# Optimization experiments

Hardware: AMD Instinct MI355X
Metric: run time of the kernel (lower is better)

Reference implementation:

```python
import jax, jax.numpy as jnp
import numpy as np

N_HEAD, N_KV, HEAD_DIM, GATE_CH = 16, 4, 128, 32

def _rope(x, cos, sin):
    d = x.shape[3] // 2
    x1, x2 = x[..., :d], x[..., d:]
    return jnp.concatenate([x1 * cos + x2 * sin, x1 * (-sin) + x2 * cos], axis=3)

def _rmsnorm(x):
    xf = x.astype(jnp.float32)
    return (x * jax.lax.rsqrt(jnp.mean(xf * xf, axis=-1, keepdims=True) + 1e-6)).astype(x.dtype)

def setup_inputs() -> dict:
    key = jax.random.key(0)
    ks = jax.random.split(key, 9)
    B, T, C = 2, 2048, 2048
    return {
        "x":  jax.random.normal(ks[0], (B, T, C), jnp.float32),
        "ve": jax.random.normal(ks[1], (B, T, N_KV * HEAD_DIM), jnp.float32),
        "cos": jax.random.uniform(ks[2], (T, 1, HEAD_DIM // 2), jnp.float32),
        "sin": jax.random.uniform(ks[3], (T, 1, HEAD_DIM // 2), jnp.float32),
        "Wq": jax.random.normal(ks[4], (C, N_HEAD * HEAD_DIM), jnp.float32) * 0.02,
        "Wk": jax.random.normal(ks[5], (C, N_KV * HEAD_DIM), jnp.float32) * 0.02,
        "Wv": jax.random.normal(ks[6], (C, N_KV * HEAD_DIM), jnp.float32) * 0.02,
        "Wg": jax.random.normal(ks[7], (GATE_CH, N_KV), jnp.float32) * 0.02,
        "Wo": jax.random.normal(ks[8], (C, C), jnp.float32) * 0.02,
        "window": 1024,
    }

def reference(x, ve, cos, sin, Wq, Wk, Wv, Wg, Wo, window):
    B, T, C = x.shape
    q = (x @ Wq).reshape(B, T, N_HEAD, HEAD_DIM)
    k = (x @ Wk).reshape(B, T, N_KV, HEAD_DIM)
    v = (x @ Wv).reshape(B, T, N_KV, HEAD_DIM)
    # value-embedding gate (ve_gate active for this layer)
    gate = 2.0 * jax.nn.sigmoid(x[..., :GATE_CH] @ Wg)  # (B,T,N_KV)
    v = v + gate[..., None] * ve.reshape(B, T, N_KV, HEAD_DIM)
    q, k = _rope(q, cos, sin), _rope(k, cos, sin)
    q, k = _rmsnorm(q), _rmsnorm(k)
    # GQA: repeat kv heads (repeat_interleave over head dim)
    groups = N_HEAD // N_KV
    k = jnp.repeat(k, groups, axis=2)
    v = jnp.repeat(v, groups, axis=2)
    scale = 1.0 / np.sqrt(HEAD_DIM)
    scores = jnp.einsum("bthd,bshd->bhts", q, k) * scale  # (B,H,T,T)
    idx = jnp.arange(T)
    diff = idx[None, :] - idx[:, None]  # diff[i,j] = j - i, as in torch code
    mask = (diff >= 0) & (diff < window)
    scores = jnp.where(mask[None, None], scores, -jnp.inf)
    p = jax.nn.softmax(scores, axis=-1)
    y = jnp.einsum("bhts,bshd->bthd", p, v).reshape(B, T, C)
    return y @ Wo
```

## Files before the change

### kernel.cpp

```cpp
#include <hip/hip_runtime.h>
#include <hip/hip_bf16.h>
#include <cstdint>

typedef __hip_bfloat16 bf16;
typedef __attribute__((ext_vector_type(8))) short short8;
typedef __attribute__((ext_vector_type(4))) float f32x4;

#define T_   2048
#define CDIM 2048
#define NH   16
#define NKV  4
#define HD   128
#define QSCALE (0.08838834764831845f * 1.44269504088896340f)

__device__ __forceinline__ void gload_lds16(const void* g, void* l) {
  __builtin_amdgcn_global_load_lds(
      (const __attribute__((address_space(1))) void*)g,
      (__attribute__((address_space(3))) void*)l, 16, 0, 0);
}

__global__ __launch_bounds__(256) void cast_x_kernel(const float4* __restrict__ in,
                                                     ushort4* __restrict__ out, int n4) {
  int i = blockIdx.x * 256 + threadIdx.x;
  if (i >= n4) return;
  float4 v = in[i];
  union { bf16 h[4]; ushort4 u; } cv;
  cv.h[0] = __float2bfloat16(v.x);
  cv.h[1] = __float2bfloat16(v.y);
  cv.h[2] = __float2bfloat16(v.z);
  cv.h[3] = __float2bfloat16(v.w);
  out[i] = cv.u;
}

__global__ __launch_bounds__(256) void cast_transpose(const float* __restrict__ W,
                                                      bf16* __restrict__ WT,
                                                      int K, int N) {
  __shared__ float tile[32][33];
  int k0 = blockIdx.y * 32, n0 = blockIdx.x * 32;
  int r = threadIdx.x >> 5, c = threadIdx.x & 31;
  for (int i = 0; i < 4; ++i)
    tile[r + i * 8][c] = W[(size_t)(k0 + r + i * 8) * N + n0 + c];
  __syncthreads();
  for (int i = 0; i < 4; ++i)
    WT[(size_t)(n0 + r + i * 8) * K + k0 + c] = __float2bfloat16(tile[c][r + i * 8]);
}

__global__ __launch_bounds__(512, 2) void gemm_qkv8(const bf16* __restrict__ A,
                                                    const bf16* __restrict__ BT,
                                                    bf16* __restrict__ C,
                                                    int N, int K, int RY, int RX) {
  __shared__ __align__(16) bf16 sA[2][256 * 64];
  __shared__ __align__(16) bf16 sB[2][256 * 64];

  int tid = threadIdx.x;
  int lane = tid & 63, w = tid >> 6;
  int wm = w >> 2, wn = w & 3;
  int lr = lane & 15, lk = lane >> 4;

  int xcd = blockIdx.x & 7, t = blockIdx.x >> 3;
  int by = (xcd >> 1) * RY + t / RX;
  int bx = (xcd & 1) * RX + t % RX;
  int m0 = by * 256, n0 = bx * 256;

  f32x4 acc[8][4];
#pragma unroll
  for (int m = 0; m < 8; ++m)
#pragma unroll
    for (int n = 0; n < 4; ++n) acc[m][n] = (f32x4){0.f, 0.f, 0.f, 0.f};

  const bf16* Abase = A + (size_t)m0 * K;
  const bf16* Bbase = BT + (size_t)n0 * K;

  auto stageB = [&](int p, int kt) {
    int kb = kt << 6;
#pragma unroll
    for (int i = 0; i < 4; ++i) {
      int c = i * 512 + tid;
      int r = c >> 3, sl = c & 7;
      gload_lds16(Bbase + (size_t)r * K + kb + ((sl ^ (r & 7)) << 3),
                  (char*)(&sB[p][0]) + c * 16);
    }
  };
  auto stageAq = [&](int p, int kt, int q) {
    int kb = kt << 6;
    int rbase = 32 * q + ((w & 3) << 3) + ((w >> 2) << 7);
    int r = rbase + (lane >> 3), sl = lane & 7;
    gload_lds16(Abase + (size_t)r * K + kb + ((sl ^ (r & 7)) << 3),
                (char*)(&sA[p][0]) + rbase * 128 + lane * 16);
  };

  int nk = K >> 6;
  stageB(0, 0);
  stageAq(0, 0, 0); stageAq(0, 0, 1); stageAq(0, 0, 2); stageAq(0, 0, 3);
  stageB(1, 1);
  stageAq(1, 1, 0); stageAq(1, 1, 1); stageAq(1, 1, 2);
  asm volatile("s_waitcnt vmcnt(7)" ::: "memory");
  __builtin_amdgcn_s_barrier();

#define READ_A(Q)                                                          \
  {                                                                        \
    _Pragma("unroll")                                                      \
    for (int mi = 0; mi < 2; ++mi) {                                       \
      int row = wm * 128 + (2 * (Q) + mi) * 16 + lr;                       \
      const char* rb = sAb + row * 128;                                    \
      int rx = (row & 7) << 4;                                             \
      af[mi][0] = *(const short8*)(rb + ((lk * 16) ^ rx));                 \
      af[mi][1] = *(const short8*)(rb + ((64 + lk * 16) ^ rx));            \
    }                                                                      \
  }
#define MFMA_Q(Q)                                                          \
  __builtin_amdgcn_s_setprio(1);                                          \
  _Pragma("unroll")                                                        \
  for (int kk = 0; kk < 2; ++kk)                                           \
    _Pragma("unroll")                                                      \
    for (int mi = 0; mi < 2; ++mi)                                         \
      _Pragma("unroll")                                                    \
      for (int n = 0; n < 4; ++n)                                          \
        acc[2 * (Q) + mi][n] = __builtin_amdgcn_mfma_f32_16x16x32_bf16(    \
            af[mi][kk], bfr[n][kk], acc[2 * (Q) + mi][n], 0, 0, 0);        \
  __builtin_amdgcn_s_setprio(0);
#define LGKM_FENCE                                                         \
  asm volatile("s_waitcnt lgkmcnt(0)" ::: "memory");                       \
  __builtin_amdgcn_sched_barrier(0);

  for (int kt = 0; kt < nk; ++kt) {
    int p = kt & 1;
    const char* sAb = (const char*)(&sA[p][0]);
    const char* sBb = (const char*)(&sB[p][0]);
    short8 bfr[4][2], af[2][2];

#pragma unroll
    for (int n = 0; n < 4; ++n) {
      int row = wn * 64 + n * 16 + lr;
      const char* rb = sBb + row * 128;
      int rx = (row & 7) << 4;
      bfr[n][0] = *(const short8*)(rb + ((lk * 16) ^ rx));
      bfr[n][1] = *(const short8*)(rb + ((64 + lk * 16) ^ rx));
    }
    READ_A(0);
    if (kt + 1 < nk) stageAq(p ^ 1, kt + 1, 3);
    LGKM_FENCE;
    MFMA_Q(0);
    __builtin_amdgcn_s_barrier();

    READ_A(1);
    if (kt + 2 < nk) { stageB(p, kt + 2); stageAq(p, kt + 2, 0); }
    LGKM_FENCE;
    MFMA_Q(1);
    __builtin_amdgcn_s_barrier();

    READ_A(2);
    if (kt + 2 < nk) stageAq(p, kt + 2, 1);
    LGKM_FENCE;
    MFMA_Q(2);
    __builtin_amdgcn_s_barrier();

    READ_A(3);
    if (kt + 2 < nk) stageAq(p, kt + 2, 2);
    LGKM_FENCE;
    MFMA_Q(3);
    if (kt + 2 < nk)
      asm volatile("s_waitcnt vmcnt(7)" ::: "memory");
    else
      asm volatile("s_waitcnt vmcnt(0)" ::: "memory");
    __builtin_amdgcn_s_barrier();
  }
#undef READ_A
#undef MFMA_Q
#undef LGKM_FENCE

#pragma unroll
  for (int m = 0; m < 8; ++m)
#pragma unroll
    for (int n = 0; n < 4; ++n)
#pragma unroll
      for (int jj = 0; jj < 4; ++jj)
        C[(size_t)(m0 + wm * 128 + m * 16 + lk * 4 + jj) * N +
          n0 + wn * 64 + n * 16 + lr] = __float2bfloat16(acc[m][n][jj]);
}

template <int MREP, typename CT>
__global__ __launch_bounds__(512, 2) void gemm_8p(const bf16* __restrict__ A,
                                                  const bf16* __restrict__ BT,
                                                  CT* __restrict__ C,
                                                  int N, int K, int RY, int RX) {
  constexpr int BM = MREP * 32;
  constexpr int ALOADS = BM / 64;
  __shared__ __align__(16) bf16 sA[2][BM * 64];
  __shared__ __align__(16) bf16 sB[2][256 * 64];

  int tid = threadIdx.x;
  int lane = tid & 63, w = tid >> 6;
  int wm = w >> 2, wn = w & 3;
  int lr = lane & 15, lk = lane >> 4;

  int xcd = blockIdx.x & 7, t = blockIdx.x >> 3;
  int by = (xcd >> 1) * RY + t / RX;
  int bx = (xcd & 1) * RX + t % RX;
  int m0 = by * BM, n0 = bx * 256;

  f32x4 acc[MREP][4];
#pragma unroll
  for (int m = 0; m < MREP; ++m)
#pragma unroll
    for (int n = 0; n < 4; ++n) acc[m][n] = (f32x4){0.f, 0.f, 0.f, 0.f};

  const bf16* Abase = A + (size_t)m0 * K;
  const bf16* Bbase = BT + (size_t)n0 * K;

  auto stage = [&](int b, int kt) {
    int kb = kt << 6;
#pragma unroll
    for (int i = 0; i < ALOADS; ++i) {
      int c = i * 512 + tid;
      int r = c >> 3, sl = c & 7;
      gload_lds16(Abase + (size_t)r * K + kb + ((sl ^ (r & 7)) << 3),
                  (char*)(&sA[b][0]) + c * 16);
    }
#pragma unroll
    for (int i = 0; i < 4; ++i) {
      int c = i * 512 + tid;
      int r = c >> 3, sl = c & 7;
      gload_lds16(Bbase + (size_t)r * K + kb + ((sl ^ (r & 7)) << 3),
                  (char*)(&sB[b][0]) + c * 16);
    }
  };

  int nk = K >> 6;
  stage(0, 0);
  stage(1, 1);
  asm volatile("s_waitcnt vmcnt(6)" ::: "memory");
  __builtin_amdgcn_s_barrier();

  for (int kt = 0; kt < nk; ++kt) {
    int d = kt & 1;
    const char* sAb = (const char*)(&sA[d][0]);
    const char* sBb = (const char*)(&sB[d][0]);

    short8 bfr[4][2];
#pragma unroll
    for (int n = 0; n < 4; ++n) {
      int row = wn * 64 + n * 16 + lr;
      const char* rb = sBb + row * 128;
      int rx = (row & 7) << 4;
      bfr[n][0] = *(const short8*)(rb + ((lk * 16) ^ rx));
      bfr[n][1] = *(const short8*)(rb + ((64 + lk * 16) ^ rx));
    }

#pragma unroll
    for (int p = 0; p < MREP / 2; ++p) {
      short8 af[2][2];
#pragma unroll
      for (int mi = 0; mi < 2; ++mi) {
        int row = wm * (MREP * 16) + (p * 2 + mi) * 16 + lr;
        const char* rb = sAb + row * 128;
        int rx = (row & 7) << 4;
        af[mi][0] = *(const short8*)(rb + ((lk * 16) ^ rx));
        af[mi][1] = *(const short8*)(rb + ((64 + lk * 16) ^ rx));
      }
      __builtin_amdgcn_s_setprio(1);
#pragma unroll
      for (int kk = 0; kk < 2; ++kk)
#pragma unroll
        for (int mi = 0; mi < 2; ++mi)
#pragma unroll
          for (int n = 0; n < 4; ++n)
            acc[p * 2 + mi][n] = __builtin_amdgcn_mfma_f32_16x16x32_bf16(
                af[mi][kk], bfr[n][kk], acc[p * 2 + mi][n], 0, 0, 0);
      __builtin_amdgcn_s_setprio(0);
    }

    asm volatile("s_waitcnt lgkmcnt(0)\n\ts_barrier" ::: "memory");
    if (kt + 2 < nk) {
      stage(d, kt + 2);
      asm volatile("s_waitcnt vmcnt(6)\n\ts_barrier" ::: "memory");
    } else {
      asm volatile("s_waitcnt vmcnt(0)\n\ts_barrier" ::: "memory");
    }
  }

#pragma unroll
  for (int m = 0; m < MREP; ++m)
#pragma unroll
    for (int n = 0; n < 4; ++n)
#pragma unroll
      for (int jj = 0; jj < 4; ++jj) {
        size_t idx = (size_t)(m0 + wm * (MREP * 16) + m * 16 + lk * 4 + jj) * N +
                     n0 + wn * 64 + n * 16 + lr;
        if constexpr (__is_same(CT, float))
          C[idx] = acc[m][n][jj];
        else
          C[idx] = __float2bfloat16(acc[m][n][jj]);
      }
}

__global__ __launch_bounds__(256) void epilogue_kernel(
    const bf16* __restrict__ qkv, const float* __restrict__ x,
    const float* __restrict__ ve, const float* __restrict__ cosT,
    const float* __restrict__ sinT, const float* __restrict__ Wg,
    bf16* __restrict__ qn, bf16* __restrict__ kn, bf16* __restrict__ vT) {
  int row = blockIdx.x;
  int bi = row >> 11, t = row & 2047;
  int tid = threadIdx.x, lane = tid & 63, w = tid >> 6;
  __shared__ float gate[NKV];
  size_t rb = (size_t)row * 3072;

  if (tid < 128) {
    int g = tid >> 5, i = tid & 31;
    float p = x[(size_t)row * CDIM + i] * Wg[i * 4 + g];
    p += __shfl_xor(p, 1);  p += __shfl_xor(p, 2);
    p += __shfl_xor(p, 4);  p += __shfl_xor(p, 8);
    p += __shfl_xor(p, 16);
    if (i == 0) gate[g] = 2.f / (1.f + __expf(-p));
  }
  __syncthreads();

  float cv = cosT[t * 64 + lane];
  float sv = sinT[t * 64 + lane];

  for (int it = 0; it < 4; ++it) {
    int h = it * 4 + w;
    float x1 = __bfloat162float(qkv[rb + h * 128 + lane]);
    float x2 = __bfloat162float(qkv[rb + h * 128 + 64 + lane]);
    float y1 = x1 * cv + x2 * sv;
    float y2 = x2 * cv - x1 * sv;
    float ss = y1 * y1 + y2 * y2;
    ss += __shfl_xor(ss, 1);  ss += __shfl_xor(ss, 2);  ss += __shfl_xor(ss, 4);
    ss += __shfl_xor(ss, 8);  ss += __shfl_xor(ss, 16); ss += __shfl_xor(ss, 32);
    float r = rsqrtf(ss * (1.f / 128.f) + 1e-6f) * QSCALE;
    size_t ob = (size_t)row * (NH * HD) + h * 128;
    qn[ob + lane] = __float2bfloat16(y1 * r);
    qn[ob + 64 + lane] = __float2bfloat16(y2 * r);
  }
  {
    int h = w;
    float x1 = __bfloat162float(qkv[rb + 2048 + h * 128 + lane]);
    float x2 = __bfloat162float(qkv[rb + 2048 + h * 128 + 64 + lane]);
    float y1 = x1 * cv + x2 * sv;
    float y2 = x2 * cv - x1 * sv;
    float ss = y1 * y1 + y2 * y2;
    ss += __shfl_xor(ss, 1);  ss += __shfl_xor(ss, 2);  ss += __shfl_xor(ss, 4);
    ss += __shfl_xor(ss, 8);  ss += __shfl_xor(ss, 16); ss += __shfl_xor(ss, 32);
    float r = rsqrtf(ss * (1.f / 128.f) + 1e-6f);
    size_t ob = (size_t)row * (NKV * HD) + h * 128;
    kn[ob + lane] = __float2bfloat16(y1 * r);
    kn[ob + 64 + lane] = __float2bfloat16(y2 * r);
  }
  for (int e = tid; e < 512; e += 256) {
    int kv = e >> 7, d = e & 127;
    float val = __bfloat162float(qkv[rb + 2560 + e]) + gate[kv] * ve[(size_t)row * 512 + e];
    vT[((size_t)(bi * NKV + kv) * HD + d) * T_ + t] = __float2bfloat16(val);
  }
}

__global__ __launch_bounds__(256) void attn_kernel(
    const bf16* __restrict__ qn, const bf16* __restrict__ kn,
    const bf16* __restrict__ vT, bf16* __restrict__ y,
    const int* __restrict__ winp) {
  __shared__ __align__(16) bf16 sK[2][64 * 128];
  __shared__ __align__(16) bf16 sV[2][128 * 64];
  __shared__ __align__(16) bf16 sP[4][16 * 64];

  int win = *winp;
  int id = blockIdx.x;
  int g  = id & 7;
  int bi = g >> 2;
  int kvh = g & 3;
  int rem = id >> 3;
  int h  = kvh * 4 + (rem & 3);
  int jslot = (rem >> 2) & 7;
  int s5 = rem >> 5;
  int q0i = (s5 == 0) ? (2 * jslot) : (s5 == 1) ? (2 * jslot + 1)
          : (s5 == 2) ? (16 + jslot) : (31 - jslot);
  int q0 = q0i << 6;
  int tid = threadIdx.x;
  int lane = tid & 63, w = tid >> 6;
  int lr = lane & 15, lk = lane >> 4;

  short8 qf[4];
  {
    const bf16* qrow = qn + (size_t)(bi * T_ + q0 + w * 16 + lr) * (NH * HD) + h * HD;
    for (int c = 0; c < 4; ++c) qf[c] = *(const short8*)(qrow + c * 32 + lk * 8);
  }

  f32x4 o[8];
  for (int i = 0; i < 8; ++i) o[i] = (f32x4){0.f, 0.f, 0.f, 0.f};
  float lpart[4] = {0.f, 0.f, 0.f, 0.f};

  int jt0 = q0 >> 6;
  int hi = q0 + 62 + win; if (hi > T_ - 1) hi = T_ - 1;
  int jt1 = hi >> 6;
  const float NEGINF = -__builtin_inff();

  char* sPb = (char*)(&sP[w][0]);
  int prx = (lr & 7) << 4;

  auto stageKV = [&](int b, int jtx) {
    int j0x = jtx << 6;
    for (int i = 0; i < 4; ++i) {
      int c = i * 256 + tid;
      int r = c >> 4, sl = c & 15;
      gload_lds16(kn + (size_t)(bi * T_ + j0x + r) * (NKV * HD) + kvh * HD + ((sl ^ (r & 7)) * 8),
                  (char*)(&sK[b][0]) + c * 16);
    }
    for (int i = 0; i < 4; ++i) {
      int c = i * 256 + tid;
      int r = c >> 3, sl = c & 7;
      gload_lds16(vT + ((size_t)(bi * NKV + kvh) * HD + r) * T_ + j0x + ((sl ^ (r & 7)) * 8),
                  (char*)(&sV[b][0]) + c * 16);
    }
  };

  stageKV(0, jt0);
  __syncthreads();

  int buf = 0;
  for (int jt = jt0; jt <= jt1; ++jt) {
    int j0 = jt << 6;
    if (jt < jt1) stageKV(buf ^ 1, jt + 1);

    const char* sKb = (const char*)(&sK[buf][0]);
    const char* sVb = (const char*)(&sV[buf][0]);

    f32x4 s[4];
    for (int sub = 0; sub < 4; ++sub) s[sub] = (f32x4){0.f, 0.f, 0.f, 0.f};
    for (int sub = 0; sub < 4; ++sub) {
      int kr = sub * 16 + lr;
      int rx = (kr & 7) << 4;
      const char* rowb = sKb + kr * 256;
      for (int c = 0; c < 4; ++c) {
        short8 kf = *(const short8*)(rowb + ((c * 64 + lk * 16) ^ rx));
        s[sub] = __builtin_amdgcn_mfma_f32_16x16x32_bf16(qf[c], kf, s[sub], 0, 0, 0);
      }
    }

    bool full = (j0 >= q0 + 64) && (j0 + 64 <= q0 + win);
    int ibase = q0 + w * 16 + lk * 4;

    for (int jj = 0; jj < 4; ++jj) {
      int irow = ibase + jj;
      int pr = lk * 4 + jj;
      int pwx = (pr & 7) << 4;
      char* pb = sPb + pr * 128;
      float v0, v1, v2, v3;
      if (full) {
        v0 = s[0][jj]; v1 = s[1][jj]; v2 = s[2][jj]; v3 = s[3][jj];
      } else {
        int j = j0 + lr;
        v0 = (j >= irow && j - irow < win)           ? s[0][jj] : NEGINF;
        v1 = (j + 16 >= irow && j + 16 - irow < win) ? s[1][jj] : NEGINF;
        v2 = (j + 32 >= irow && j + 32 - irow < win) ? s[2][jj] : NEGINF;
        v3 = (j + 48 >= irow && j + 48 - irow < win) ? s[3][jj] : NEGINF;
      }
      float p0 = exp2f(v0), p1 = exp2f(v1);
      float p2 = exp2f(v2), p3 = exp2f(v3);
      lpart[jj] += (p0 + p1) + (p2 + p3);
      *(bf16*)(pb + ((lr * 2)      ^ pwx)) = __float2bfloat16(p0);
      *(bf16*)(pb + ((32 + lr * 2) ^ pwx)) = __float2bfloat16(p1);
      *(bf16*)(pb + ((64 + lr * 2) ^ pwx)) = __float2bfloat16(p2);
      *(bf16*)(pb + ((96 + lr * 2) ^ pwx)) = __float2bfloat16(p3);
    }

    short8 pf0 = *(const short8*)(sPb + lr * 128 + ((lk * 16)      ^ prx));
    short8 pf1 = *(const short8*)(sPb + lr * 128 + ((64 + lk * 16) ^ prx));
    for (int nb = 0; nb < 8; ++nb) {
      int vr = nb * 16 + lr;
      int vrx = (vr & 7) << 4;
      const char* vb = sVb + vr * 128;
      short8 vf0 = *(const short8*)(vb + ((lk * 16)      ^ vrx));
      short8 vf1 = *(const short8*)(vb + ((64 + lk * 16) ^ vrx));
      o[nb] = __builtin_amdgcn_mfma_f32_16x16x32_bf16(pf0, vf0, o[nb], 0, 0, 0);
      o[nb] = __builtin_amdgcn_mfma_f32_16x16x32_bf16(pf1, vf1, o[nb], 0, 0, 0);
    }
    __syncthreads();
    buf ^= 1;
  }

  for (int jj = 0; jj < 4; ++jj) {
    float l = lpart[jj];
    l += __shfl_xor(l, 1); l += __shfl_xor(l, 2);
    l += __shfl_xor(l, 4); l += __shfl_xor(l, 8);
    float inv = 1.f / l;
    size_t ob = (size_t)(bi * T_ + q0 + w * 16 + lk * 4 + jj) * (NH * HD) + h * HD;
    for (int nb = 0; nb < 8; ++nb)
      y[ob + nb * 16 + lr] = __float2bfloat16(o[nb][jj] * inv);
  }
}

extern "C" void kernel_launch(void* const* d_in, const int* in_sizes, int n_in,
                              void* d_out, int out_size, void* d_ws, size_t ws_size,
                              hipStream_t stream) {
  const float* x    = (const float*)d_in[0];
  const float* ve   = (const float*)d_in[1];
  const float* cosT = (const float*)d_in[2];
  const float* sinT = (const float*)d_in[3];
  const float* Wq   = (const float*)d_in[4];
  const float* Wk   = (const float*)d_in[5];
  const float* Wv   = (const float*)d_in[6];
  const float* Wg   = (const float*)d_in[7];
  const float* Wo   = (const float*)d_in[8];
  const int*   win  = (const int*)d_in[9];
  float* out = (float*)d_out;

  char* ws = (char*)d_ws;
  bf16*  xb   = (bf16*)(ws);
  bf16*  wT   = (bf16*)(ws + 16777216);
  bf16*  woT  = (bf16*)(ws + 29360128);
  bf16*  qkvb = (bf16*)(ws + 37748736);
  bf16*  qn   = (bf16*)(ws + 62914560);
  bf16*  kn   = (bf16*)(ws + 79691776);
  bf16*  vTb  = (bf16*)(ws + 83886080);
  bf16*  y    = qkvb;

  cast_x_kernel<<<8192, 256, 0, stream>>>((const float4*)x, (ushort4*)xb, 2097152);
  cast_transpose<<<dim3(64, 64), 256, 0, stream>>>(Wq, wT, 2048, 2048);
  cast_transpose<<<dim3(16, 64), 256, 0, stream>>>(Wk, wT + (size_t)2048 * 2048, 2048, 512);
  cast_transpose<<<dim3(16, 64), 256, 0, stream>>>(Wv, wT + (size_t)2560 * 2048, 2048, 512);
  cast_transpose<<<dim3(64, 64), 256, 0, stream>>>(Wo, woT, 2048, 2048);

  gemm_qkv8<<<192, 512, 0, stream>>>(xb, wT, qkvb, 3072, 2048, 4, 6);
  epilogue_kernel<<<4096, 256, 0, stream>>>(qkvb, x, ve, cosT, sinT, Wg, qn, kn, vTb);
  attn_kernel<<<1024, 256, 0, stream>>>(qn, kn, vTb, y, win);
  gemm_8p<4, float><<<256, 512, 0, stream>>>(y, woT, out, 2048, 2048, 8, 4);
}
```

Before: 212.3 us.

## Keep P in registers via transposed QK MFMA and register-staged KV prefetch

Swaps the QK^T MFMA operand order so each lane holds a transposed score fragment. Probabilities then pack directly into bf16 PV operands with v_cvt_pk_bf16_f32, which removes the per-wave LDS round trip for P. K/V staging changes from double-buffered global_load_lds to register prefetch two tiles ahead with a single LDS buffer. That halves LDS use, allowing launch_bounds occupancy 3 and s_setprio around the MFMA blocks. In exchange it needs extra barriers per tile, more registers, and a more intricate V swizzle written with split 8-byte stores.

```diff
diff --git a/kernel.cpp b/kernel.cpp
--- a/kernel.cpp
+++ b/kernel.cpp
@@ -4,6 +4,7 @@
 
 typedef __hip_bfloat16 bf16;
 typedef __attribute__((ext_vector_type(8))) short short8;
+typedef __attribute__((ext_vector_type(4))) short short4v;
 typedef __attribute__((ext_vector_type(4))) float f32x4;
 
 #define T_   2048
@@ -353,19 +354,17 @@
   }
 }
 
-__global__ __launch_bounds__(256) void attn_kernel(
+__global__ __launch_bounds__(256, 3) void attn_kernel(
     const bf16* __restrict__ qn, const bf16* __restrict__ kn,
     const bf16* __restrict__ vT, bf16* __restrict__ y,
     const int* __restrict__ winp) {
-  __shared__ __align__(16) bf16 sK[2][64 * 128];
-  __shared__ __align__(16) bf16 sV[2][128 * 64];
-  __shared__ __align__(16) bf16 sP[4][16 * 64];
+  __shared__ __align__(16) bf16 sK[64 * 128];
+  __shared__ __align__(16) bf16 sV[128 * 64];
 
   int win = *winp;
   int id = blockIdx.x;
   int g  = id & 7;
-  int bi = g >> 2;
-  int kvh = g & 3;
+  int bi = g >> 2, kvh = g & 3;
   int rem = id >> 3;
   int h  = kvh * 4 + (rem & 3);
   int jslot = (rem >> 2) & 7;
@@ -380,108 +379,140 @@
   short8 qf[4];
   {
     const bf16* qrow = qn + (size_t)(bi * T_ + q0 + w * 16 + lr) * (NH * HD) + h * HD;
+#pragma unroll
     for (int c = 0; c < 4; ++c) qf[c] = *(const short8*)(qrow + c * 32 + lk * 8);
   }
 
+  int kge[4], klb[4], vge[4], vlbA[4], vlbB[4];
+#pragma unroll
+  for (int i = 0; i < 4; ++i) {
+    int c = i * 256 + tid;
+    int kr = c >> 4, ks = c & 15;
+    kge[i] = kr * (NKV * HD) + ks * 8;
+    klb[i] = kr * 256 + ((ks ^ (kr & 7)) << 4);
+    int vr = c >> 3, vs = c & 7;
+    vge[i] = vr * T_ + vs * 8;
+    int hh = vs >> 2, m = vs & 3, a = m >> 1;
+    int sA = 8 * ((2 * m) & 3) + 4 * a;
+    int sB = 8 * ((2 * m + 1) & 3) + 4 * a;
+    int tA = 64 * hh + 2 * sA, tB = 64 * hh + 2 * sB;
+    vlbA[i] = vr * 128 + (((tA >> 4) ^ (vr & 7)) << 4) + (tA & 15);
+    vlbB[i] = vr * 128 + (((tB >> 4) ^ (vr & 7)) << 4) + (tB & 15);
+  }
+  const bf16* kpane = kn + (size_t)bi * T_ * (NKV * HD) + kvh * HD;
+  const bf16* vpane = vT + (size_t)(bi * NKV + kvh) * HD * T_;
+
+  short8 kreg[4], vreg[4];
+  auto LOAD = [&](int jtx) {
+    const bf16* kb = kpane + (size_t)(jtx << 6) * (NKV * HD);
+    const bf16* vb = vpane + (jtx << 6);
+#pragma unroll
+    for (int i = 0; i < 4; ++i) kreg[i] = *(const short8*)(kb + kge[i]);
+#pragma unroll
+    for (int i = 0; i < 4; ++i) vreg[i] = *(const short8*)(vb + vge[i]);
+  };
+  auto WRITE = [&]() {
+#pragma unroll
+    for (int i = 0; i < 4; ++i) *(short8*)((char*)sK + klb[i]) = kreg[i];
+#pragma unroll
+    for (int i = 0; i < 4; ++i) {
+      union { short8 s8; short4v s4[2]; } u;
+      u.s8 = vreg[i];
+      *(short4v*)((char*)sV + vlbA[i]) = u.s4[0];
+      *(short4v*)((char*)sV + vlbB[i]) = u.s4[1];
+    }
+  };
+
   f32x4 o[8];
+#pragma unroll
   for (int i = 0; i < 8; ++i) o[i] = (f32x4){0.f, 0.f, 0.f, 0.f};
-  float lpart[4] = {0.f, 0.f, 0.f, 0.f};
+  float lpart = 0.f;
 
   int jt0 = q0 >> 6;
   int hi = q0 + 62 + win; if (hi > T_ - 1) hi = T_ - 1;
   int jt1 = hi >> 6;
-  const float NEGINF = -__builtin_inff();
-
-  char* sPb = (char*)(&sP[w][0]);
-  int prx = (lr & 7) << 4;
-
-  auto stageKV = [&](int b, int jtx) {
-    int j0x = jtx << 6;
-    for (int i = 0; i < 4; ++i) {
-      int c = i * 256 + tid;
-      int r = c >> 4, sl = c & 15;
-      gload_lds16(kn + (size_t)(bi * T_ + j0x + r) * (NKV * HD) + kvh * HD + ((sl ^ (r & 7)) * 8),
-                  (char*)(&sK[b][0]) + c * 16);
-    }
-    for (int i = 0; i < 4; ++i) {
-      int c = i * 256 + tid;
-      int r = c >> 3, sl = c & 7;
-      gload_lds16(vT + ((size_t)(bi * NKV + kvh) * HD + r) * T_ + j0x + ((sl ^ (r & 7)) * 8),
-                  (char*)(&sV[b][0]) + c * 16);
-    }
-  };
-
-  stageKV(0, jt0);
-  __syncthreads();
-
-  int buf = 0;
+
+  LOAD(jt0);
+  WRITE();
+  if (jt0 < jt1) LOAD(jt0 + 1);
+  asm volatile("s_waitcnt lgkmcnt(0)\n\ts_barrier" ::: "memory");
+
+  int irow = q0 + w * 16 + lr;
+  int klo = lk * 4;
+
   for (int jt = jt0; jt <= jt1; ++jt) {
     int j0 = jt << 6;
-    if (jt < jt1) stageKV(buf ^ 1, jt + 1);
-
-    const char* sKb = (const char*)(&sK[buf][0]);
-    const char* sVb = (const char*)(&sV[buf][0]);
 
     f32x4 s[4];
+#pragma unroll
     for (int sub = 0; sub < 4; ++sub) s[sub] = (f32x4){0.f, 0.f, 0.f, 0.f};
+    __builtin_amdgcn_s_setprio(1);
+#pragma unroll
     for (int sub = 0; sub < 4; ++sub) {
       int kr = sub * 16 + lr;
       int rx = (kr & 7) << 4;
-      const char* rowb = sKb + kr * 256;
+      const char* rowb = (const char*)sK + kr * 256;
+#pragma unroll
       for (int c = 0; c < 4; ++c) {
         short8 kf = *(const short8*)(rowb + ((c * 64 + lk * 16) ^ rx));
-        s[sub] = __builtin_amdgcn_mfma_f32_16x16x32_bf16(qf[c], kf, s[sub], 0, 0, 0);
+        s[sub] = __builtin_amdgcn_mfma_f32_16x16x32_bf16(kf, qf[c], s[sub], 0, 0, 0);
       }
     }
+    __builtin_amdgcn_s_setprio(0);
 
     bool full = (j0 >= q0 + 64) && (j0 + 64 <= q0 + win);
-    int ibase = q0 + w * 16 + lk * 4;
-
-    for (int jj = 0; jj < 4; ++jj) {
-      int irow = ibase + jj;
-      int pr = lk * 4 + jj;
-      int pwx = (pr & 7) << 4;
-      char* pb = sPb + pr * 128;
-      float v0, v1, v2, v3;
-      if (full) {
-        v0 = s[0][jj]; v1 = s[1][jj]; v2 = s[2][jj]; v3 = s[3][jj];
-      } else {
-        int j = j0 + lr;
-        v0 = (j >= irow && j - irow < win)           ? s[0][jj] : NEGINF;
-        v1 = (j + 16 >= irow && j + 16 - irow < win) ? s[1][jj] : NEGINF;
-        v2 = (j + 32 >= irow && j + 32 - irow < win) ? s[2][jj] : NEGINF;
-        v3 = (j + 48 >= irow && j + 48 - irow < win) ? s[3][jj] : NEGINF;
+    int koff = j0 - irow;
+
+    unsigned pk[8];
+#pragma unroll
+    for (int sub = 0; sub < 4; ++sub) {
+      float p0 = exp2f(s[sub][0]), p1 = exp2f(s[sub][1]);
+      float p2 = exp2f(s[sub][2]), p3 = exp2f(s[sub][3]);
+      if (!full) {
+        int base = koff + sub * 16 + klo;
+        p0 = ((unsigned)(base + 0) < (unsigned)win) ? p0 : 0.f;
+        p1 = ((unsigned)(base + 1) < (unsigned)win) ? p1 : 0.f;
+        p2 = ((unsigned)(base + 2) < (unsigned)win) ? p2 : 0.f;
+        p3 = ((unsigned)(base + 3) < (unsigned)win) ? p3 : 0.f;
       }
-      float p0 = exp2f(v0), p1 = exp2f(v1);
-      float p2 = exp2f(v2), p3 = exp2f(v3);
-      lpart[jj] += (p0 + p1) + (p2 + p3);
-      *(bf16*)(pb + ((lr * 2)      ^ pwx)) = __float2bfloat16(p0);
-      *(bf16*)(pb + ((32 + lr * 2) ^ pwx)) = __float2bfloat16(p1);
-      *(bf16*)(pb + ((64 + lr * 2) ^ pwx)) = __float2bfloat16(p2);
-      *(bf16*)(pb + ((96 + lr * 2) ^ pwx)) = __float2bfloat16(p3);
-    }
-
-    short8 pf0 = *(const short8*)(sPb + lr * 128 + ((lk * 16)      ^ prx));
-    short8 pf1 = *(const short8*)(sPb + lr * 128 + ((64 + lk * 16) ^ prx));
+      lpart += (p0 + p1) + (p2 + p3);
+      asm("v_cvt_pk_bf16_f32 %0, %1, %2" : "=v"(pk[sub * 2])     : "v"(p0), "v"(p1));
+      asm("v_cvt_pk_bf16_f32 %0, %1, %2" : "=v"(pk[sub * 2 + 1]) : "v"(p2), "v"(p3));
+    }
+    union { unsigned u[4]; short8 s8; } c0, c1;
+    c0.u[0] = pk[0]; c0.u[1] = pk[1]; c0.u[2] = pk[2]; c0.u[3] = pk[3];
+    c1.u[0] = pk[4]; c1.u[1] = pk[5]; c1.u[2] = pk[6]; c1.u[3] = pk[7];
+    short8 pf0 = c0.s8, pf1 = c1.s8;
+
+    __builtin_amdgcn_s_setprio(1);
+#pragma unroll
     for (int nb = 0; nb < 8; ++nb) {
       int vr = nb * 16 + lr;
       int vrx = (vr & 7) << 4;
-      const char* vb = sVb + vr * 128;
-      short8 vf0 = *(const short8*)(vb + ((lk * 16)      ^ vrx));
+      const char* vb = (const char*)sV + vr * 128;
+      short8 vf0 = *(const short8*)(vb + ((lk * 16) ^ vrx));
       short8 vf1 = *(const short8*)(vb + ((64 + lk * 16) ^ vrx));
       o[nb] = __builtin_amdgcn_mfma_f32_16x16x32_bf16(pf0, vf0, o[nb], 0, 0, 0);
       o[nb] = __builtin_amdgcn_mfma_f32_16x16x32_bf16(pf1, vf1, o[nb], 0, 0, 0);
     }
-    __syncthreads();
-    buf ^= 1;
-  }
-
+    __builtin_amdgcn_s_setprio(0);
+
+    asm volatile("s_waitcnt lgkmcnt(0)\n\ts_barrier" ::: "memory");
+    if (jt < jt1) {
+      WRITE();
+      if (jt + 1 < jt1) LOAD(jt + 2);
+      asm volatile("s_waitcnt lgkmcnt(0)\n\ts_barrier" ::: "memory");
+    }
+  }
+
+  float l = lpart;
+  l += __shfl_xor(l, 16);
+  l += __shfl_xor(l, 32);
+#pragma unroll
   for (int jj = 0; jj < 4; ++jj) {
-    float l = lpart[jj];
-    l += __shfl_xor(l, 1); l += __shfl_xor(l, 2);
-    l += __shfl_xor(l, 4); l += __shfl_xor(l, 8);
-    float inv = 1.f / l;
-    size_t ob = (size_t)(bi * T_ + q0 + w * 16 + lk * 4 + jj) * (NH * HD) + h * HD;
+    float inv = 1.f / __shfl(l, klo + jj);
+    size_t ob = (size_t)(bi * T_ + q0 + w * 16 + klo + jj) * (NH * HD) + h * HD;
+#pragma unroll
     for (int nb = 0; nb < 8; ++nb)
       y[ob + nb * 16 + lr] = __float2bfloat16(o[nb][jj] * inv);
   }
```

Result: faster. 200.9 us (-5.4%).
